# Kernel optimization log

Measured on AMD Instinct MI355X. Metric: run time of the kernel, lower is better.

## Reference

```python
import jax, jax.numpy as jnp
import numpy as np


def setup_inputs() -> dict:
    key = jax.random.key(0)
    k1, k2 = jax.random.split(key)
    B, IN, OUT = 4096, 4096, 4096
    x = jax.random.normal(k1, (B, IN), dtype=jnp.float32)
    W = jax.random.normal(k2, (OUT, IN), dtype=jnp.float32) * (1.0 / np.sqrt(IN))
    return {"x": x, "W": W, "k": 128}


def reference(x, W, k):
    # temp = (x[:, None, :] * W).sum(axis=1)  ==  x * W.sum(axis=0)  -> [B, in]
    # (the original materializes the O(B*out*in) intermediate; math is identical)
    temp = jax.lax.stop_gradient(x) * jnp.sum(W, axis=0)  # x_vals is detached in torch
    _, idx_top = jax.lax.top_k(jnp.abs(temp), k)          # [B, k] indices into `in` dim
    B = x.shape[0]
    z = jnp.ones_like(x).at[jnp.arange(B)[:, None], idx_top].set(0.0)
    out = jnp.matmul(x * z, W.T)                          # [B, out]
    return out
```

## Files before the change

### kernel.cpp

```cpp
#include <hip/hip_runtime.h>
#include <hip/hip_bf16.h>
#include <stdint.h>

#define B_DIM   4096
#define IN_DIM  4096
#define OUT_DIM 4096
#define K_SEL   128

typedef unsigned short u16;
typedef __bf16 bf16x8 __attribute__((ext_vector_type(8)));
typedef float  f32x4  __attribute__((ext_vector_type(4)));

static __device__ __forceinline__ u16 f2bf(float f) {
    uint32_t u = __builtin_bit_cast(uint32_t, f);
    uint32_t r = (u + 0x7fffu + ((u >> 16) & 1u)) >> 16;
    return (u16)r;
}

__global__ __launch_bounds__(256) void colsum_conv(const float* __restrict__ W,
                                                   double* __restrict__ part,
                                                   u16* __restrict__ Wb) {
    int cb = blockIdx.x & 3;
    int rb = blockIdx.x >> 2;
    int c4 = cb * 256 + threadIdx.x;
    int row0 = rb * 8;
    double s0 = 0.0, s1 = 0.0, s2 = 0.0, s3 = 0.0;
    for (int r = 0; r < 8; ++r) {
        const float4 v = ((const float4*)(W + (size_t)(row0 + r) * IN_DIM))[c4];
        s0 += (double)v.x; s1 += (double)v.y; s2 += (double)v.z; s3 += (double)v.w;
        ushort4 o;
        o.x = f2bf(v.x); o.y = f2bf(v.y); o.z = f2bf(v.z); o.w = f2bf(v.w);
        ((ushort4*)(Wb + (size_t)(row0 + r) * IN_DIM))[c4] = o;
    }
    double4 d; d.x = s0; d.y = s1; d.z = s2; d.w = s3;
    ((double4*)(part + (size_t)rb * IN_DIM))[c4] = d;
}

__global__ __launch_bounds__(256) void colsum_final(const double* __restrict__ part,
                                                    float* __restrict__ cs) {
    int col = blockIdx.x * 256 + threadIdx.x;
    double s = 0.0;
    for (int r = 0; r < 512; ++r) s += part[(size_t)r * IN_DIM + col];
    cs[col] = (float)s;
}

__global__ __launch_bounds__(256) void topk_mask(const float* __restrict__ x,
                                                 const float* __restrict__ cs,
                                                 u16* __restrict__ xz) {
    __shared__ uint32_t hist[256];
    __shared__ uint32_t suf[256];
    __shared__ uint32_t s_scan[256];
    __shared__ uint32_t s_prefix, s_krem;

    const int b = blockIdx.x, t = threadIdx.x;
    const float4* xrow = (const float4*)(x + (size_t)b * IN_DIM);
    const float4* csv  = (const float4*)cs;

    float    xr[16];
    uint32_t ul[16];
#pragma unroll
    for (int q = 0; q < 4; ++q) {
        float4 xv = xrow[t * 4 + q];
        float4 cv = csv[t * 4 + q];
        xr[q*4+0] = xv.x; xr[q*4+1] = xv.y; xr[q*4+2] = xv.z; xr[q*4+3] = xv.w;
        ul[q*4+0] = __builtin_bit_cast(uint32_t, xv.x * cv.x) & 0x7fffffffu;
        ul[q*4+1] = __builtin_bit_cast(uint32_t, xv.y * cv.y) & 0x7fffffffu;
        ul[q*4+2] = __builtin_bit_cast(uint32_t, xv.z * cv.z) & 0x7fffffffu;
        ul[q*4+3] = __builtin_bit_cast(uint32_t, xv.w * cv.w) & 0x7fffffffu;
    }
    if (t == 0) { s_prefix = 0u; s_krem = K_SEL; }
    __syncthreads();

#pragma unroll
    for (int p = 3; p >= 0; --p) {
        const int sh = p * 8;
        const uint32_t hi_mask = (p == 3) ? 0u : (0xFFFFFFFFu << (sh + 8));
        const uint32_t prefix = s_prefix;
        const uint32_t krem   = s_krem;
        hist[t] = 0u;
        __syncthreads();
#pragma unroll
        for (int j = 0; j < 16; ++j) {
            uint32_t u = ul[j];
            if ((u & hi_mask) == (prefix & hi_mask))
                atomicAdd(&hist[(u >> sh) & 255u], 1u);
        }
        __syncthreads();
        uint32_t mine = hist[t];
        suf[t] = mine;
        __syncthreads();
#pragma unroll
        for (int off = 1; off < 256; off <<= 1) {
            uint32_t other = (t + off < 256) ? suf[t + off] : 0u;
            __syncthreads();
            mine += other;
            suf[t] = mine;
            __syncthreads();
        }
        uint32_t mysuf   = suf[t];
        uint32_t nextsuf = (t < 255) ? suf[t + 1] : 0u;
        if (mysuf >= krem && (t == 255 || nextsuf < krem)) {
            s_prefix = prefix | ((uint32_t)t << sh);
            s_krem   = krem - nextsuf;
        }
        __syncthreads();
    }
    const uint32_t T       = s_prefix;
    const uint32_t need_eq = s_krem;

    int cnt = 0;
#pragma unroll
    for (int j = 0; j < 16; ++j) cnt += (ul[j] == T) ? 1 : 0;
    s_scan[t] = (uint32_t)cnt;
    __syncthreads();
    uint32_t inc = (uint32_t)cnt;
#pragma unroll
    for (int off = 1; off < 256; off <<= 1) {
        uint32_t other = (t >= off) ? s_scan[t - off] : 0u;
        __syncthreads();
        inc += other;
        s_scan[t] = inc;
        __syncthreads();
    }
    const int base = (int)(inc - (uint32_t)cnt);

    union { u16 us[16]; uint4 v[2]; } ob;
    int eqseen = 0;
#pragma unroll
    for (int j = 0; j < 16; ++j) {
        uint32_t u = ul[j];
        bool drop = (u > T);
        if (u == T) {
            if (base + eqseen < (int)need_eq) drop = true;
            ++eqseen;
        }
        ob.us[j] = drop ? (u16)0 : f2bf(xr[j]);
    }
    uint4* dst = (uint4*)(xz + (size_t)b * IN_DIM + t * 16);
    dst[0] = ob.v[0];
    dst[1] = ob.v[1];
}

#define NT 64

__global__ __launch_bounds__(512, 2) void gemm_pl(const u16* __restrict__ A,
                                                  const u16* __restrict__ Bm,
                                                  float* __restrict__ C) {
    __shared__ u16 lds_[65536];

    const int bid = blockIdx.x;
    const int swz = (bid & 7) * 32 + (bid >> 3);
    const int m0 = (swz >> 4) * 256, n0 = (swz & 15) * 256;

    const int t = threadIdx.x;
    const int l = t & 63;
    const int lr = l & 15, lk = l >> 4;
    const int w = t >> 6;
    const int wm = w >> 2, wn = w & 3;

    const int cswz = ((t & 7) ^ ((t >> 3) & 7)) * 8;
    const int c0   = (lk ^ (lr & 7)) * 8;
    const int c1   = c0 ^ 32;

    f32x4 acc[8][4];
#pragma unroll
    for (int i = 0; i < 8; ++i)
#pragma unroll
        for (int j = 0; j < 4; ++j) acc[i][j] = f32x4{0.f, 0.f, 0.f, 0.f};

#define GLOAD(g, off_bytes)                                                     \
    __builtin_amdgcn_global_load_lds(                                           \
        (const __attribute__((address_space(1))) void*)(g),                     \
        (__attribute__((address_space(3))) void*)(((char*)lds_) + (off_bytes)), \
        16, 0, 0)

    auto stA = [&](int kb, int qm, int kt) {
#pragma unroll
        for (int g = 0; g < 2; ++g)
            GLOAD(A + (size_t)(m0 + g * 128 + qm * 64 + (t >> 3)) * IN_DIM + kt + cswz,
                  kb * 65536 + qm * 16384 + g * 8192 + t * 16);
    };
    auto stB = [&](int kb, int qn, int kt) {
#pragma unroll
        for (int g = 0; g < 2; ++g)
            GLOAD(Bm + (size_t)(n0 + (g * 2 + (t >> 8)) * 64 + qn * 32 + ((t >> 3) & 31)) * IN_DIM + kt + cswz,
                  kb * 65536 + 32768 + qn * 16384 + g * 8192 + t * 16);
    };

    auto rdA = [&](bf16x8 (&dst)[4], int bufo, int qm, int c) {
#pragma unroll
        for (int mi = 0; mi < 4; ++mi)
            dst[mi] = *(const bf16x8*)&lds_[bufo + qm * 8192 + wm * 4096 + lr * 64 + mi * 1024 + c];
    };
    auto rdB = [&](bf16x8 (&dst)[4], int bufo, int c) {
#pragma unroll
        for (int ni = 0; ni < 4; ++ni)
            dst[ni] = *(const bf16x8*)&lds_[bufo + 16384 + (ni >> 1) * 8192 + wn * 2048 + lr * 64 + (ni & 1) * 1024 + c];
    };
    auto mm = [&](int base, bf16x8 (&Aa)[4], bf16x8 (&Bb)[4]) {
#pragma unroll
        for (int mi = 0; mi < 4; ++mi)
#pragma unroll
            for (int ni = 0; ni < 4; ++ni)
                acc[base + mi][ni] = __builtin_amdgcn_mfma_f32_16x16x32_bf16(
                    Aa[mi], Bb[ni], acc[base + mi][ni], 0, 0, 0);
    };

    bf16x8 aX[4], aY[4], bX[4], bY[4];

    stA(0, 0, 0); stA(0, 1, 0); stB(0, 0, 0); stB(0, 1, 0);
    asm volatile("s_waitcnt vmcnt(0)" ::: "memory");
    __builtin_amdgcn_s_barrier();
    asm volatile("" ::: "memory");
    rdA(aX, 0, 0, c0);
    rdB(bX, 0, c0);

    for (int k = 0; k < NT; ++k) {
        const int bufo = (k & 1) * 32768, bufno = bufo ^ 32768;
        const int kbn  = (k & 1) ^ 1;
        const int kt1  = (k + 1) * 64;

        rdA(aY, bufo, 1, c0);
        if (k < NT - 1) {
            stA(kbn, 0, kt1); stA(kbn, 1, kt1);
            stB(kbn, 0, kt1); stB(kbn, 1, kt1);
        }
        __builtin_amdgcn_s_setprio(1);
        mm(0, aX, bX);
        __builtin_amdgcn_s_setprio(0);
        __builtin_amdgcn_sched_barrier(0);

        rdA(aX, bufo, 0, c1);
        rdB(bY, bufo, c1);
        __builtin_amdgcn_s_setprio(1);
        mm(4, aY, bX);
        __builtin_amdgcn_s_setprio(0);
        __builtin_amdgcn_sched_barrier(0);

        rdA(aY, bufo, 1, c1);
        __builtin_amdgcn_s_setprio(1);
        mm(0, aX, bY);
        __builtin_amdgcn_s_setprio(0);
        __builtin_amdgcn_sched_barrier(0);
        asm volatile("s_waitcnt vmcnt(0)" ::: "memory");
        __builtin_amdgcn_s_barrier();
        asm volatile("" ::: "memory");

        if (k < NT - 1) {
            rdA(aX, bufno, 0, c0);
            rdB(bX, bufno, c0);
        }
        __builtin_amdgcn_s_setprio(1);
        mm(4, aY, bY);
        __builtin_amdgcn_s_setprio(0);
        __builtin_amdgcn_sched_barrier(0);
        asm volatile("" ::: "memory");
        __builtin_amdgcn_s_barrier();
        asm volatile("" ::: "memory");
    }
#undef GLOAD

#pragma unroll
    for (int gmi = 0; gmi < 8; ++gmi)
#pragma unroll
        for (int ni = 0; ni < 4; ++ni)
#pragma unroll
            for (int r = 0; r < 4; ++r) {
                int row = m0 + wm * 128 + (gmi >> 2) * 64 + (gmi & 3) * 16 + lk * 4 + r;
                int col = n0 + wn * 64 + ni * 16 + lr;
                C[(size_t)row * OUT_DIM + col] = acc[gmi][ni][r];
            }
}

extern "C" void kernel_launch(void* const* d_in, const int* in_sizes, int n_in,
                              void* d_out, int out_size, void* d_ws, size_t ws_size,
                              hipStream_t stream) {
    const float* x = (const float*)d_in[0];
    const float* W = (const float*)d_in[1];
    float* out = (float*)d_out;

    char* ws = (char*)d_ws;
    u16*    Wb   = (u16*)ws;
    u16*    xz   = (u16*)(ws + (size_t)32 * 1024 * 1024);
    float*  cs   = (float*)(ws + (size_t)64 * 1024 * 1024);
    double* part = (double*)d_out;

    colsum_conv<<<2048, 256, 0, stream>>>(W, part, Wb);
    colsum_final<<<16, 256, 0, stream>>>(part, cs);
    topk_mask<<<4096, 256, 0, stream>>>(x, cs, xz);
    gemm_pl<<<256, 512, 0, stream>>>(xz, Wb, out);
}
```

Measured before the change: 204.3 us.

## Prefetch GEMM tiles two steps ahead with staggered quarter loads; parallelize colsum reduction

```diff
diff --git a/kernel.cpp b/kernel.cpp
--- a/kernel.cpp
+++ b/kernel.cpp
@@ -38,10 +38,19 @@
 
 __global__ __launch_bounds__(256) void colsum_final(const double* __restrict__ part,
                                                     float* __restrict__ cs) {
-    int col = blockIdx.x * 256 + threadIdx.x;
+    __shared__ double red[256];
+    const int t = threadIdx.x;
+    const int c = blockIdx.x * 16 + (t & 15);
+    const int g = t >> 4;
     double s = 0.0;
-    for (int r = 0; r < 512; ++r) s += part[(size_t)r * IN_DIM + col];
-    cs[col] = (float)s;
+    for (int r = 0; r < 32; ++r) s += part[(size_t)(g * 32 + r) * IN_DIM + c];
+    red[t] = s;
+    __syncthreads();
+    for (int off = 128; off >= 16; off >>= 1) {
+        if (t < off) red[t] += red[t + off];
+        __syncthreads();
+    }
+    if (t < 16) cs[blockIdx.x * 16 + t] = (float)red[t];
 }
 
 __global__ __launch_bounds__(256) void topk_mask(const float* __restrict__ x,
@@ -174,17 +183,17 @@
         (__attribute__((address_space(3))) void*)(((char*)lds_) + (off_bytes)), \
         16, 0, 0)
 
-    auto stA = [&](int kb, int qm, int kt) {
+    auto stA = [&](int kb, int r, int kt) {
 #pragma unroll
         for (int g = 0; g < 2; ++g)
-            GLOAD(A + (size_t)(m0 + g * 128 + qm * 64 + (t >> 3)) * IN_DIM + kt + cswz,
-                  kb * 65536 + qm * 16384 + g * 8192 + t * 16);
-    };
-    auto stB = [&](int kb, int qn, int kt) {
+            GLOAD(A + (size_t)(m0 + g * 128 + r * 64 + (t >> 3)) * IN_DIM + kt + cswz,
+                  kb * 65536 + r * 16384 + g * 8192 + t * 16);
+    };
+    auto stB = [&](int kb, int r, int kt) {
 #pragma unroll
         for (int g = 0; g < 2; ++g)
-            GLOAD(Bm + (size_t)(n0 + (g * 2 + (t >> 8)) * 64 + qn * 32 + ((t >> 3) & 31)) * IN_DIM + kt + cswz,
-                  kb * 65536 + 32768 + qn * 16384 + g * 8192 + t * 16);
+            GLOAD(Bm + (size_t)(n0 + r * 128 + g * 64 + (t >> 3)) * IN_DIM + kt + cswz,
+                  kb * 65536 + 32768 + r * 16384 + g * 8192 + t * 16);
     };
 
     auto rdA = [&](bf16x8 (&dst)[4], int bufo, int qm, int c) {
@@ -195,66 +204,69 @@
     auto rdB = [&](bf16x8 (&dst)[4], int bufo, int c) {
 #pragma unroll
         for (int ni = 0; ni < 4; ++ni)
-            dst[ni] = *(const bf16x8*)&lds_[bufo + 16384 + (ni >> 1) * 8192 + wn * 2048 + lr * 64 + (ni & 1) * 1024 + c];
+            dst[ni] = *(const bf16x8*)&lds_[bufo + 16384 + (wn >> 1) * 8192 + (wn & 1) * 4096 + lr * 64 + ni * 1024 + c];
     };
     auto mm = [&](int base, bf16x8 (&Aa)[4], bf16x8 (&Bb)[4]) {
+        __builtin_amdgcn_s_setprio(1);
 #pragma unroll
         for (int mi = 0; mi < 4; ++mi)
 #pragma unroll
             for (int ni = 0; ni < 4; ++ni)
                 acc[base + mi][ni] = __builtin_amdgcn_mfma_f32_16x16x32_bf16(
                     Aa[mi], Bb[ni], acc[base + mi][ni], 0, 0, 0);
-    };
-
-    bf16x8 aX[4], aY[4], bX[4], bY[4];
+        __builtin_amdgcn_s_setprio(0);
+        __builtin_amdgcn_sched_barrier(0);
+    };
+
+    bf16x8 a0k0[4], a0k1[4], a1k0[4], a1k1[4], bk0[4], bk1[4];
 
     stA(0, 0, 0); stA(0, 1, 0); stB(0, 0, 0); stB(0, 1, 0);
-    asm volatile("s_waitcnt vmcnt(0)" ::: "memory");
+    stA(1, 0, 64); stB(1, 0, 64); stB(1, 1, 64);
+    asm volatile("s_waitcnt vmcnt(6)" ::: "memory");
     __builtin_amdgcn_s_barrier();
     asm volatile("" ::: "memory");
-    rdA(aX, 0, 0, c0);
-    rdB(bX, 0, c0);
+    rdA(a0k0, 0, 0, c0);
+    rdB(bk0, 0, c0);
 
     for (int k = 0; k < NT; ++k) {
-        const int bufo = (k & 1) * 32768, bufno = bufo ^ 32768;
-        const int kbn  = (k & 1) ^ 1;
-        const int kt1  = (k + 1) * 64;
-
-        rdA(aY, bufo, 1, c0);
-        if (k < NT - 1) {
-            stA(kbn, 0, kt1); stA(kbn, 1, kt1);
-            stB(kbn, 0, kt1); stB(kbn, 1, kt1);
-        }
-        __builtin_amdgcn_s_setprio(1);
-        mm(0, aX, bX);
-        __builtin_amdgcn_s_setprio(0);
-        __builtin_amdgcn_sched_barrier(0);
-
-        rdA(aX, bufo, 0, c1);
-        rdB(bY, bufo, c1);
-        __builtin_amdgcn_s_setprio(1);
-        mm(4, aY, bX);
-        __builtin_amdgcn_s_setprio(0);
-        __builtin_amdgcn_sched_barrier(0);
-
-        rdA(aY, bufo, 1, c1);
-        __builtin_amdgcn_s_setprio(1);
-        mm(0, aX, bY);
-        __builtin_amdgcn_s_setprio(0);
-        __builtin_amdgcn_sched_barrier(0);
-        asm volatile("s_waitcnt vmcnt(0)" ::: "memory");
+        const int bufo = (k & 1) * 32768;
+        const int bufno = bufo ^ 32768;
+        const int kbC = k & 1, kbN = kbC ^ 1;
+        const int kt1 = (k + 1) * 64, kt2 = (k + 2) * 64;
+
+        rdA(a0k1, bufo, 0, c1);
+        rdB(bk1, bufo, c1);
+        if (k < NT - 1) stA(kbN, 1, kt1);
+        mm(0, a0k0, bk0);
+        asm volatile("s_waitcnt lgkmcnt(0)" ::: "memory");
         __builtin_amdgcn_s_barrier();
         asm volatile("" ::: "memory");
 
+        rdA(a1k0, bufo, 1, c0);
+        rdA(a1k1, bufo, 1, c1);
+        if (k < NT - 2) stA(kbC, 0, kt2);
+        mm(0, a0k1, bk1);
+        asm volatile("s_waitcnt lgkmcnt(0)" ::: "memory");
+        __builtin_amdgcn_s_barrier();
+        asm volatile("" ::: "memory");
+
+        if (k < NT - 2) stB(kbC, 0, kt2);
+        mm(4, a1k0, bk0);
+        if (k < NT - 2) {
+            asm volatile("s_waitcnt vmcnt(4) lgkmcnt(0)" ::: "memory");
+        } else {
+            asm volatile("s_waitcnt vmcnt(0) lgkmcnt(0)" ::: "memory");
+        }
+        __builtin_amdgcn_s_barrier();
+        asm volatile("" ::: "memory");
+
         if (k < NT - 1) {
-            rdA(aX, bufno, 0, c0);
-            rdB(bX, bufno, c0);
-        }
-        __builtin_amdgcn_s_setprio(1);
-        mm(4, aY, bY);
-        __builtin_amdgcn_s_setprio(0);
-        __builtin_amdgcn_sched_barrier(0);
-        asm volatile("" ::: "memory");
+            rdA(a0k0, bufno, 0, c0);
+            rdB(bk0, bufno, c0);
+        }
+        if (k < NT - 2) stB(kbC, 1, kt2);
+        mm(4, a1k1, bk1);
+        asm volatile("s_waitcnt lgkmcnt(0)" ::: "memory");
         __builtin_amdgcn_s_barrier();
         asm volatile("" ::: "memory");
     }
@@ -286,7 +298,7 @@
     double* part = (double*)d_out;
 
     colsum_conv<<<2048, 256, 0, stream>>>(W, part, Wb);
-    colsum_final<<<16, 256, 0, stream>>>(part, cs);
+    colsum_final<<<256, 256, 0, stream>>>(part, cs);
     topk_mask<<<4096, 256, 0, stream>>>(x, cs, xz);
     gemm_pl<<<256, 512, 0, stream>>>(xz, Wb, out);
 }
```

Result: faster. 188.7 us (-7.7%).
